# Optimization experiments

Hardware: AMD Instinct MI355X
Metric: run time of the kernel (lower is better)

## Reference

```python
import jax, jax.numpy as jnp
import numpy as np

B, N, T, L = 4, 512, 288, 128
NEG_SLOPE = 0.2
TEMPERATURE = 0.2
CLAMP = 10.0
EPS = 1e-10


def setup_inputs() -> dict:
    key = jax.random.key(0)
    ks = jax.random.split(key, 6)
    s_in = 1.0 / np.sqrt(T)
    s_lat = 1.0 / np.sqrt(2 * L)
    s_b = 1.0 / np.sqrt(L)
    x = jax.random.normal(ks[0], (B, N, T), dtype=jnp.float32)
    W1 = jax.random.normal(ks[1], (L, T), dtype=jnp.float32) * s_in
    W2 = jax.random.normal(ks[2], (L, T), dtype=jnp.float32) * s_in
    Wp = jax.random.normal(ks[3], (L, 2 * L), dtype=jnp.float32) * s_lat
    Wb = jax.random.normal(ks[4], (L,), dtype=jnp.float32) * s_b
    noise = jnp.clip(jax.random.uniform(ks[5], (N, N), dtype=jnp.float32), 1e-6, 1.0 - 1e-6)
    return {
        "x": x,
        "W1": W1, "b1": jnp.zeros((L,), jnp.float32),
        "W2": W2, "b2": jnp.zeros((L,), jnp.float32),
        "Wp": Wp, "bp": jnp.zeros((L,), jnp.float32),
        "Wb": Wb, "bb": jnp.zeros((1,), jnp.float32),
        "noise": noise,
    }


def _leaky(v):
    return jnp.where(v >= 0, v, NEG_SLOPE * v)


def reference(x, W1, b1, W2, b2, Wp, bp, Wb, bb, noise):
    # per-node projections (B, N, L)
    x1 = _leaky(jnp.einsum('bnt,lt->bnl', x, W1) + b1)
    x2 = _leaky(jnp.einsum('bnt,lt->bnl', x, W2) + b2)
    # linear_para_latent(cat(x1_i, x2_j)) == x1_i @ Wp_a^T + x2_j @ Wp_b^T + bp
    Wp_a, Wp_b = Wp[:, :L], Wp[:, L:]
    s1 = jnp.einsum('bnl,ml->bnm', x1, Wp_a)  # (B, N, L_out)
    s2 = jnp.einsum('bnl,ml->bnm', x2, Wp_b)
    pair = s1[:, :, None, :] + s2[:, None, :, :] + bp  # (B, N, N, L)
    h = _leaky(pair)
    logits = jnp.einsum('bijl,l->bij', h, Wb) + bb[0]  # (B, N, N)
    p = jax.nn.sigmoid(logits).mean(axis=0)            # (N, N)
    p = p * (1.0 - jnp.eye(N, dtype=p.dtype))          # fill_diagonal_(0)
    # relaxed Bernoulli sample (binary concrete) with logit clamping
    logit_p = jnp.clip(jnp.log(p + EPS) - jnp.log1p(-p + EPS), -CLAMP, CLAMP)
    logistic = jnp.log(noise) - jnp.log1p(-noise)
    adj = jax.nn.sigmoid((logit_p + logistic) / TEMPERATURE)
    return adj
```

## Files before the change

### kernel.cpp

```cpp
#include <hip/hip_runtime.h>
#include <hip/hip_bf16.h>
#include <math.h>

#define NN 512
#define NT 288

__global__ __launch_bounds__(256) void kT(
    const float* __restrict__ W1, const float* __restrict__ W2,
    const float* __restrict__ Wp,
    float* __restrict__ Wt, float* __restrict__ Wpt)
{
    int g = blockIdx.x * 256 + threadIdx.x;
    if (g < 288 * 256) {
        int k = g >> 8, col = g & 255;
        Wt[g] = (col < 128) ? W1[col * 288 + k] : W2[(col - 128) * 288 + k];
    } else {
        int h = g - 288 * 256;
        int k = h >> 8, col = h & 255;
        Wpt[h] = (col < 128) ? Wp[col * 256 + k]
                             : Wp[(col - 128) * 256 + 128 + k];
    }
}

__global__ __launch_bounds__(512, 4) void kP(
    const float* __restrict__ x,
    const float* __restrict__ Wt,
    const float* __restrict__ b1,
    const float* __restrict__ b2,
    const float* __restrict__ Wpt,
    const float* __restrict__ bp,
    const float* __restrict__ Wb,
    const float* __restrict__ bb,
    float* __restrict__ S12,
    float* __restrict__ Aarr,
    float* __restrict__ Carr)
{
    __shared__ __align__(16) float xs[4 * NT];
    __shared__ __align__(16) float x12s[4 * 256];
    __shared__ __align__(16) float ph[7 * 1024];
    __shared__ __align__(16) float s12s[4 * 260];

    const int t   = threadIdx.x;
    const int bn0 = blockIdx.x * 4;
    const int c4  = t & 63;
    const int khe = t >> 6;

    if (t < 288) {
        int row = t / 72, cc = t % 72;
        *(float4*)&xs[row * NT + cc * 4] =
            *(const float4*)&x[(size_t)(bn0 + row) * NT + cc * 4];
    }
    __syncthreads();

    float acc[4][4];
#pragma unroll
    for (int n = 0; n < 4; ++n)
#pragma unroll
        for (int c = 0; c < 4; ++c) acc[n][c] = 0.0f;

    const int kbase1 = khe * 36;
#pragma unroll 2
    for (int k4 = 0; k4 < 9; ++k4) {
        const int k0 = kbase1 + k4 * 4;
        float4 w0 = *(const float4*)&Wt[(size_t)(k0 + 0) * 256 + c4 * 4];
        float4 w1 = *(const float4*)&Wt[(size_t)(k0 + 1) * 256 + c4 * 4];
        float4 w2 = *(const float4*)&Wt[(size_t)(k0 + 2) * 256 + c4 * 4];
        float4 w3 = *(const float4*)&Wt[(size_t)(k0 + 3) * 256 + c4 * 4];
        const float* w0p = (const float*)&w0;
        const float* w1p = (const float*)&w1;
        const float* w2p = (const float*)&w2;
        const float* w3p = (const float*)&w3;
#pragma unroll
        for (int n = 0; n < 4; ++n) {
            float4 xv = *(const float4*)&xs[n * NT + k0];
#pragma unroll
            for (int c = 0; c < 4; ++c) {
                acc[n][c] = fmaf(xv.x, w0p[c], acc[n][c]);
                acc[n][c] = fmaf(xv.y, w1p[c], acc[n][c]);
                acc[n][c] = fmaf(xv.z, w2p[c], acc[n][c]);
                acc[n][c] = fmaf(xv.w, w3p[c], acc[n][c]);
            }
        }
    }

    if (khe) {
#pragma unroll
        for (int n = 0; n < 4; ++n) {
            float4 v = {acc[n][0], acc[n][1], acc[n][2], acc[n][3]};
            *(float4*)&ph[(khe - 1) * 1024 + n * 256 + c4 * 4] = v;
        }
    }
    __syncthreads();
    if (!khe) {
        float4 bias4 = (c4 < 32) ? *(const float4*)&b1[c4 * 4]
                                 : *(const float4*)&b2[(c4 - 32) * 4];
        const float* bp4 = (const float*)&bias4;
#pragma unroll
        for (int n = 0; n < 4; ++n) {
            float s0 = acc[n][0], s1 = acc[n][1], s2 = acc[n][2], s3 = acc[n][3];
#pragma unroll
            for (int p = 0; p < 7; ++p) {
                float4 v = *(const float4*)&ph[p * 1024 + n * 256 + c4 * 4];
                s0 += v.x; s1 += v.y; s2 += v.z; s3 += v.w;
            }
            float sv[4] = {s0, s1, s2, s3};
            float4 r;
            float* rp = (float*)&r;
#pragma unroll
            for (int c = 0; c < 4; ++c) {
                float v = sv[c] + bp4[c];
                rp[c] = fmaxf(v, 0.2f * v);
            }
            *(float4*)&x12s[n * 256 + c4 * 4] = r;
        }
    }
    __syncthreads();

    float acc2[4][4];
#pragma unroll
    for (int n = 0; n < 4; ++n)
#pragma unroll
        for (int c = 0; c < 4; ++c) acc2[n][c] = 0.0f;

    const int koff = (c4 < 32) ? 0 : 128;
    const int kbase2 = khe * 16;
#pragma unroll 2
    for (int k4 = 0; k4 < 4; ++k4) {
        const int k0 = kbase2 + k4 * 4;
        float4 w0 = *(const float4*)&Wpt[(size_t)(k0 + 0) * 256 + c4 * 4];
        float4 w1 = *(const float4*)&Wpt[(size_t)(k0 + 1) * 256 + c4 * 4];
        float4 w2 = *(const float4*)&Wpt[(size_t)(k0 + 2) * 256 + c4 * 4];
        float4 w3 = *(const float4*)&Wpt[(size_t)(k0 + 3) * 256 + c4 * 4];
        const float* w0p = (const float*)&w0;
        const float* w1p = (const float*)&w1;
        const float* w2p = (const float*)&w2;
        const float* w3p = (const float*)&w3;
#pragma unroll
        for (int n = 0; n < 4; ++n) {
            float4 xv = *(const float4*)&x12s[n * 256 + koff + k0];
#pragma unroll
            for (int c = 0; c < 4; ++c) {
                acc2[n][c] = fmaf(xv.x, w0p[c], acc2[n][c]);
                acc2[n][c] = fmaf(xv.y, w1p[c], acc2[n][c]);
                acc2[n][c] = fmaf(xv.z, w2p[c], acc2[n][c]);
                acc2[n][c] = fmaf(xv.w, w3p[c], acc2[n][c]);
            }
        }
    }

    if (khe) {
#pragma unroll
        for (int n = 0; n < 4; ++n) {
            float4 v = {acc2[n][0], acc2[n][1], acc2[n][2], acc2[n][3]};
            *(float4*)&ph[(khe - 1) * 1024 + n * 256 + c4 * 4] = v;
        }
    }
    __syncthreads();
    if (!khe) {
        float4 bias4;
        if (c4 < 32) bias4 = *(const float4*)&bp[c4 * 4];
        else         bias4 = make_float4(0.f, 0.f, 0.f, 0.f);
        const float* bp4 = (const float*)&bias4;
#pragma unroll
        for (int n = 0; n < 4; ++n) {
            float s0 = acc2[n][0], s1 = acc2[n][1], s2 = acc2[n][2], s3 = acc2[n][3];
#pragma unroll
            for (int p = 0; p < 7; ++p) {
                float4 v = *(const float4*)&ph[p * 1024 + n * 256 + c4 * 4];
                s0 += v.x; s1 += v.y; s2 += v.z; s3 += v.w;
            }
            float sv[4] = {s0, s1, s2, s3};
            float4 r;
            float* rp = (float*)&r;
#pragma unroll
            for (int c = 0; c < 4; ++c) rp[c] = sv[c] + bp4[c];
            *(float4*)&S12[(size_t)(bn0 + n) * 256 + c4 * 4] = r;
            *(float4*)&s12s[n * 260 + c4 * 4] = r;
        }
    }
    __syncthreads();

    {
        int lane = t & 63;
        int d = t >> 6;
        int n = d & 3;
        int isC = d >> 2;
        int base = isC ? 128 : 0;
        float sum = fmaf(s12s[n * 260 + base + lane], Wb[lane],
                         s12s[n * 260 + base + lane + 64] * Wb[lane + 64]);
#pragma unroll
        for (int m = 32; m >= 1; m >>= 1)
            sum += __shfl_xor(sum, m, 64);
        if (lane == 0) {
            if (isC) Carr[bn0 + n] = 0.6f * sum;
            else     Aarr[bn0 + n] = 0.6f * sum + bb[0];
        }
    }
}

__global__ __launch_bounds__(512) void kQ(
    const float* __restrict__ S12,
    const float* __restrict__ Aarr,
    const float* __restrict__ Carr,
    const float* __restrict__ Wb,
    const float* __restrict__ noise,
    float* __restrict__ out)
{
    __shared__ __align__(16) float smem[32768];
    float* S1t = smem;
    float* S2t = smem + 16384;

    const int t = threadIdx.x;
    const int bx = blockIdx.x, by = blockIdx.y;

#pragma unroll
    for (int q = 0; q < 16; ++q) {
        int task = q * 512 + t;
        int isS2 = task >> 12;
        int r    = task & 4095;
        int bz   = r >> 10;
        int row  = (r >> 5) & 31;
        int c4   = r & 31;
        size_t src = (size_t)(bz * NN + (isS2 ? by : bx) * 32 + row) * 256
                     + (isS2 ? 128 : 0) + c4 * 4;
        float4 v = *(const float4*)&S12[src];
        float* dst = (isS2 ? S2t : S1t) + bz * 4096;
        int rw = row ^ ((c4 & 7) << 2);
        dst[(c4 * 4 + 0) * 32 + rw] = v.x;
        dst[(c4 * 4 + 1) * 32 + rw] = v.y;
        dst[(c4 * 4 + 2) * 32 + rw] = v.z;
        dst[(c4 * 4 + 3) * 32 + rw] = v.w;
    }
    __syncthreads();

    const int lh = t >> 8;
    const int bz = (t >> 6) & 3;
    const int s  = t & 63;
    const int i0 = (s >> 3) << 2, j0 = (s & 7) << 2;

    const float* S1b = S1t + bz * 4096 + lh * 64 * 32;
    const float* S2b = S2t + bz * 4096 + lh * 64 * 32;
    const float* wbp = Wb + lh * 64;

    float accv[16];
#pragma unroll
    for (int k = 0; k < 16; ++k) accv[k] = 0.0f;

    for (int l4 = 0; l4 < 16; ++l4) {
        const int sw = (l4 & 7) << 2;
        const int lrow = l4 * 4 * 32;
        float4 wv = *(const float4*)&wbp[l4 * 4];
        const float wl[4] = {wv.x, wv.y, wv.z, wv.w};
#pragma unroll
        for (int d = 0; d < 4; ++d) {
            float4 a = *(const float4*)&S1b[lrow + d * 32 + (i0 ^ sw)];
            float4 b = *(const float4*)&S2b[lrow + d * 32 + (j0 ^ sw)];
            float w = wl[d];
            float ai[4] = {a.x, a.y, a.z, a.w};
            float bj[4] = {b.x, b.y, b.z, b.w};
#pragma unroll
            for (int ii = 0; ii < 4; ++ii)
#pragma unroll
                for (int jj = 0; jj < 4; ++jj) {
                    float tv = ai[ii] + bj[jj];
                    accv[ii * 4 + jj] = fmaf(fabsf(tv), w, accv[ii * 4 + jj]);
                }
        }
    }

    float* red = smem;
    const int tid2 = t & 255;
    __syncthreads();
    if (lh) {
#pragma unroll
        for (int q = 0; q < 4; ++q) {
            float4 v = {accv[4 * q], accv[4 * q + 1], accv[4 * q + 2], accv[4 * q + 3]};
            *(float4*)&red[q * 1024 + tid2 * 4] = v;
        }
    }
    __syncthreads();

    float sig[16];
    if (!lh) {
#pragma unroll
        for (int q = 0; q < 4; ++q) {
            float4 v = *(const float4*)&red[q * 1024 + tid2 * 4];
            accv[4 * q]     += v.x;
            accv[4 * q + 1] += v.y;
            accv[4 * q + 2] += v.z;
            accv[4 * q + 3] += v.w;
        }
        float Av[4], Cv[4];
#pragma unroll
        for (int ii = 0; ii < 4; ++ii) Av[ii] = Aarr[bz * NN + bx * 32 + i0 + ii];
#pragma unroll
        for (int jj = 0; jj < 4; ++jj) Cv[jj] = Carr[bz * NN + by * 32 + j0 + jj];
#pragma unroll
        for (int ii = 0; ii < 4; ++ii)
#pragma unroll
            for (int jj = 0; jj < 4; ++jj) {
                float lg = Av[ii] + Cv[jj] + 0.4f * accv[ii * 4 + jj];
                sig[ii * 4 + jj] = 1.0f / (1.0f + expf(-lg));
            }
        float* redB = smem + 4096;
        if (bz) {
#pragma unroll
            for (int q = 0; q < 4; ++q) {
                float4 v = {sig[4 * q], sig[4 * q + 1], sig[4 * q + 2], sig[4 * q + 3]};
                *(float4*)&redB[(bz - 1) * 1024 + q * 256 + s * 4] = v;
            }
        }
    }
    __syncthreads();

    float* redB = smem + 4096;
    float* redP = smem + 7168;
    if (t < 64) {
#pragma unroll
        for (int bzz = 0; bzz < 3; ++bzz)
#pragma unroll
            for (int q = 0; q < 4; ++q) {
                float4 v = *(const float4*)&redB[bzz * 1024 + q * 256 + t * 4];
                sig[4 * q]     += v.x;
                sig[4 * q + 1] += v.y;
                sig[4 * q + 2] += v.z;
                sig[4 * q + 3] += v.w;
            }
#pragma unroll
        for (int q = 0; q < 4; ++q) {
            float4 v = {sig[4 * q], sig[4 * q + 1], sig[4 * q + 2], sig[4 * q + 3]};
            *(float4*)&redP[t * 16 + q * 4] = v;
        }
    }
    __syncthreads();

    if (t < 256) {
        int i   = t >> 3;
        int j0f = (t & 7) * 4;
        int sP  = (t >> 5) * 8 + (t & 7);
        int k0  = ((t >> 3) & 3) * 4;
        float4 pv4 = *(const float4*)&redP[sP * 16 + k0];
        float pv[4] = {pv4.x, pv4.y, pv4.z, pv4.w};

        int gi = bx * 32 + i;
        size_t base = (size_t)gi * NN + by * 32 + j0f;
        float4 nz = *(const float4*)&noise[base];
        float nv[4] = {nz.x, nz.y, nz.z, nz.w};

        float4 o;
        float* op = (float*)&o;
#pragma unroll
        for (int c = 0; c < 4; ++c) {
            float p = 0.25f * pv[c];
            int gj = by * 32 + j0f + c;
            if (gj == gi) p = 0.0f;
            float lp = logf(p + 1e-10f) - log1pf(-p + 1e-10f);
            lp = fminf(fmaxf(lp, -10.0f), 10.0f);
            float lgs = logf(nv[c]) - log1pf(-nv[c]);
            op[c] = 1.0f / (1.0f + expf(-(lp + lgs) * 5.0f));
        }
        *(float4*)&out[base] = o;
    }
}

extern "C" void kernel_launch(void* const* d_in, const int* in_sizes, int n_in,
                              void* d_out, int out_size, void* d_ws, size_t ws_size,
                              hipStream_t stream) {
    const float* x     = (const float*)d_in[0];
    const float* W1    = (const float*)d_in[1];
    const float* b1    = (const float*)d_in[2];
    const float* W2    = (const float*)d_in[3];
    const float* b2    = (const float*)d_in[4];
    const float* Wp    = (const float*)d_in[5];
    const float* bp    = (const float*)d_in[6];
    const float* Wb    = (const float*)d_in[7];
    const float* bb    = (const float*)d_in[8];
    const float* noise = (const float*)d_in[9];

    float* ws   = (float*)d_ws;
    float* S12  = ws;
    float* Aarr = ws + 524288;
    float* Carr = Aarr + 2048;
    float* Wt   = Carr + 2048;
    float* Wpt  = Wt + 73728;

    kT<<<416, 256, 0, stream>>>(W1, W2, Wp, Wt, Wpt);
    kP<<<512, 512, 0, stream>>>(x, Wt, b1, b2, Wpt, bp, Wb, bb,
                                S12, Aarr, Carr);
    kQ<<<dim3(16, 16), 512, 0, stream>>>(S12, Aarr, Carr, Wb, noise,
                                         (float*)d_out);
}
```

Baseline: 38.81 us.

## Halve kP block size and software-prefetch weight tiles in projection loops

```diff
diff --git a/kernel.cpp b/kernel.cpp
--- a/kernel.cpp
+++ b/kernel.cpp
@@ -22,7 +22,7 @@
     }
 }
 
-__global__ __launch_bounds__(512, 4) void kP(
+__global__ __launch_bounds__(256, 4) void kP(
     const float* __restrict__ x,
     const float* __restrict__ Wt,
     const float* __restrict__ b1,
@@ -37,18 +37,21 @@
 {
     __shared__ __align__(16) float xs[4 * NT];
     __shared__ __align__(16) float x12s[4 * 256];
-    __shared__ __align__(16) float ph[7 * 1024];
+    __shared__ __align__(16) float ph[3 * 1024];
     __shared__ __align__(16) float s12s[4 * 260];
 
     const int t   = threadIdx.x;
     const int bn0 = blockIdx.x * 4;
     const int c4  = t & 63;
-    const int khe = t >> 6;
-
-    if (t < 288) {
-        int row = t / 72, cc = t % 72;
-        *(float4*)&xs[row * NT + cc * 4] =
-            *(const float4*)&x[(size_t)(bn0 + row) * NT + cc * 4];
+    const int kq  = t >> 6;
+
+    for (int q = 0; q < 2; ++q) {
+        int idx = q * 256 + t;
+        if (idx < 288) {
+            int row = idx / 72, cc = idx % 72;
+            *(float4*)&xs[row * NT + cc * 4] =
+                *(const float4*)&x[(size_t)(bn0 + row) * NT + cc * 4];
+        }
     }
     __syncthreads();
 
@@ -58,18 +61,29 @@
 #pragma unroll
         for (int c = 0; c < 4; ++c) acc[n][c] = 0.0f;
 
-    const int kbase1 = khe * 36;
-#pragma unroll 2
-    for (int k4 = 0; k4 < 9; ++k4) {
-        const int k0 = kbase1 + k4 * 4;
-        float4 w0 = *(const float4*)&Wt[(size_t)(k0 + 0) * 256 + c4 * 4];
-        float4 w1 = *(const float4*)&Wt[(size_t)(k0 + 1) * 256 + c4 * 4];
-        float4 w2 = *(const float4*)&Wt[(size_t)(k0 + 2) * 256 + c4 * 4];
-        float4 w3 = *(const float4*)&Wt[(size_t)(k0 + 3) * 256 + c4 * 4];
-        const float* w0p = (const float*)&w0;
-        const float* w1p = (const float*)&w1;
-        const float* w2p = (const float*)&w2;
-        const float* w3p = (const float*)&w3;
+    const int kb1 = kq * 72;
+    const float* wcol = Wt + (size_t)kb1 * 256 + c4 * 4;
+
+    float4 cw0 = *(const float4*)&wcol[0];
+    float4 cw1 = *(const float4*)&wcol[256];
+    float4 cw2 = *(const float4*)&wcol[512];
+    float4 cw3 = *(const float4*)&wcol[768];
+
+#pragma unroll 1
+    for (int s = 0; s < 18; ++s) {
+        float4 nw0, nw1, nw2, nw3;
+        if (s < 17) {
+            const float* wn = wcol + (size_t)(s + 1) * 1024;
+            nw0 = *(const float4*)&wn[0];
+            nw1 = *(const float4*)&wn[256];
+            nw2 = *(const float4*)&wn[512];
+            nw3 = *(const float4*)&wn[768];
+        }
+        const int k0 = kb1 + s * 4;
+        const float* w0p = (const float*)&cw0;
+        const float* w1p = (const float*)&cw1;
+        const float* w2p = (const float*)&cw2;
+        const float* w3p = (const float*)&cw3;
 #pragma unroll
         for (int n = 0; n < 4; ++n) {
             float4 xv = *(const float4*)&xs[n * NT + k0];
@@ -81,17 +95,18 @@
                 acc[n][c] = fmaf(xv.w, w3p[c], acc[n][c]);
             }
         }
-    }
-
-    if (khe) {
+        if (s < 17) { cw0 = nw0; cw1 = nw1; cw2 = nw2; cw3 = nw3; }
+    }
+
+    if (kq) {
 #pragma unroll
         for (int n = 0; n < 4; ++n) {
             float4 v = {acc[n][0], acc[n][1], acc[n][2], acc[n][3]};
-            *(float4*)&ph[(khe - 1) * 1024 + n * 256 + c4 * 4] = v;
-        }
-    }
-    __syncthreads();
-    if (!khe) {
+            *(float4*)&ph[(kq - 1) * 1024 + n * 256 + c4 * 4] = v;
+        }
+    }
+    __syncthreads();
+    if (!kq) {
         float4 bias4 = (c4 < 32) ? *(const float4*)&b1[c4 * 4]
                                  : *(const float4*)&b2[(c4 - 32) * 4];
         const float* bp4 = (const float*)&bias4;
@@ -99,7 +114,7 @@
         for (int n = 0; n < 4; ++n) {
             float s0 = acc[n][0], s1 = acc[n][1], s2 = acc[n][2], s3 = acc[n][3];
 #pragma unroll
-            for (int p = 0; p < 7; ++p) {
+            for (int p = 0; p < 3; ++p) {
                 float4 v = *(const float4*)&ph[p * 1024 + n * 256 + c4 * 4];
                 s0 += v.x; s1 += v.y; s2 += v.z; s3 += v.w;
             }
@@ -123,18 +138,29 @@
         for (int c = 0; c < 4; ++c) acc2[n][c] = 0.0f;
 
     const int koff = (c4 < 32) ? 0 : 128;
-    const int kbase2 = khe * 16;
-#pragma unroll 2
-    for (int k4 = 0; k4 < 4; ++k4) {
-        const int k0 = kbase2 + k4 * 4;
-        float4 w0 = *(const float4*)&Wpt[(size_t)(k0 + 0) * 256 + c4 * 4];
-        float4 w1 = *(const float4*)&Wpt[(size_t)(k0 + 1) * 256 + c4 * 4];
-        float4 w2 = *(const float4*)&Wpt[(size_t)(k0 + 2) * 256 + c4 * 4];
-        float4 w3 = *(const float4*)&Wpt[(size_t)(k0 + 3) * 256 + c4 * 4];
-        const float* w0p = (const float*)&w0;
-        const float* w1p = (const float*)&w1;
-        const float* w2p = (const float*)&w2;
-        const float* w3p = (const float*)&w3;
+    const int kb2 = kq * 32;
+    const float* wpcol = Wpt + (size_t)kb2 * 256 + c4 * 4;
+
+    float4 dw0 = *(const float4*)&wpcol[0];
+    float4 dw1 = *(const float4*)&wpcol[256];
+    float4 dw2 = *(const float4*)&wpcol[512];
+    float4 dw3 = *(const float4*)&wpcol[768];
+
+#pragma unroll 1
+    for (int s = 0; s < 8; ++s) {
+        float4 nw0, nw1, nw2, nw3;
+        if (s < 7) {
+            const float* wn = wpcol + (size_t)(s + 1) * 1024;
+            nw0 = *(const float4*)&wn[0];
+            nw1 = *(const float4*)&wn[256];
+            nw2 = *(const float4*)&wn[512];
+            nw3 = *(const float4*)&wn[768];
+        }
+        const int k0 = kb2 + s * 4;
+        const float* w0p = (const float*)&dw0;
+        const float* w1p = (const float*)&dw1;
+        const float* w2p = (const float*)&dw2;
+        const float* w3p = (const float*)&dw3;
 #pragma unroll
         for (int n = 0; n < 4; ++n) {
             float4 xv = *(const float4*)&x12s[n * 256 + koff + k0];
@@ -146,17 +172,18 @@
                 acc2[n][c] = fmaf(xv.w, w3p[c], acc2[n][c]);
             }
         }
-    }
-
-    if (khe) {
+        if (s < 7) { dw0 = nw0; dw1 = nw1; dw2 = nw2; dw3 = nw3; }
+    }
+
+    if (kq) {
 #pragma unroll
         for (int n = 0; n < 4; ++n) {
             float4 v = {acc2[n][0], acc2[n][1], acc2[n][2], acc2[n][3]};
-            *(float4*)&ph[(khe - 1) * 1024 + n * 256 + c4 * 4] = v;
-        }
-    }
-    __syncthreads();
-    if (!khe) {
+            *(float4*)&ph[(kq - 1) * 1024 + n * 256 + c4 * 4] = v;
+        }
+    }
+    __syncthreads();
+    if (!kq) {
         float4 bias4;
         if (c4 < 32) bias4 = *(const float4*)&bp[c4 * 4];
         else         bias4 = make_float4(0.f, 0.f, 0.f, 0.f);
@@ -165,7 +192,7 @@
         for (int n = 0; n < 4; ++n) {
             float s0 = acc2[n][0], s1 = acc2[n][1], s2 = acc2[n][2], s3 = acc2[n][3];
 #pragma unroll
-            for (int p = 0; p < 7; ++p) {
+            for (int p = 0; p < 3; ++p) {
                 float4 v = *(const float4*)&ph[p * 1024 + n * 256 + c4 * 4];
                 s0 += v.x; s1 += v.y; s2 += v.z; s3 += v.w;
             }
@@ -181,17 +208,20 @@
     __syncthreads();
 
     {
-        int lane = t & 63;
-        int d = t >> 6;
-        int n = d & 3;
-        int isC = d >> 2;
+        int lane32 = t & 31;
+        int n = (t >> 5) & 3;
+        int isC = t >> 7;
         int base = isC ? 128 : 0;
-        float sum = fmaf(s12s[n * 260 + base + lane], Wb[lane],
-                         s12s[n * 260 + base + lane + 64] * Wb[lane + 64]);
-#pragma unroll
-        for (int m = 32; m >= 1; m >>= 1)
-            sum += __shfl_xor(sum, m, 64);
-        if (lane == 0) {
+        float sum = 0.0f;
+#pragma unroll
+        for (int s = 0; s < 4; ++s) {
+            int j = lane32 + s * 32;
+            sum = fmaf(s12s[n * 260 + base + j], Wb[j], sum);
+        }
+#pragma unroll
+        for (int m = 16; m >= 1; m >>= 1)
+            sum += __shfl_xor(sum, m, 32);
+        if (lane32 == 0) {
             if (isC) Carr[bn0 + n] = 0.6f * sum;
             else     Aarr[bn0 + n] = 0.6f * sum + bb[0];
         }
@@ -385,7 +415,7 @@
     float* Wpt  = Wt + 73728;
 
     kT<<<416, 256, 0, stream>>>(W1, W2, Wp, Wt, Wpt);
-    kP<<<512, 512, 0, stream>>>(x, Wt, b1, b2, Wpt, bp, Wb, bb,
+    kP<<<512, 256, 0, stream>>>(x, Wt, b1, b2, Wpt, bp, Wb, bb,
                                 S12, Aarr, Carr);
     kQ<<<dim3(16, 16), 512, 0, stream>>>(S12, Aarr, Carr, Wb, noise,
                                          (float*)d_out);
```

Measured after the change: 42.62 us. 9.8% more time.
